# Performance work log

Hardware: AMD Instinct MI355X
Metric: run time of the kernel (lower is better)

## Reference

```python
import jax, jax.numpy as jnp
import numpy as np

START_IDX = 1


def lstm_cell(x, h, c, Wih, Whh, b):
    # x:[B,Din] h,c:[B,Hc]  Wih:[4Hc,Din] Whh:[4Hc,Hc] b:[4Hc] (b_ih+b_hh combined)
    gates = x @ Wih.T + h @ Whh.T + b
    i, f, g, o = jnp.split(gates, 4, axis=-1)
    c = jax.nn.sigmoid(f) * c + jax.nn.sigmoid(i) * jnp.tanh(g)
    h = jax.nn.sigmoid(o) * jnp.tanh(c)
    return h, c


def run_lstm_dir(xs, Wih, Whh, b, h0, c0, reverse):
    # xs:[T,B,Din] -> ys:[T,B,Hc] aligned with input positions (PyTorch semantics)
    def step(carry, x):
        h, c = carry
        h, c = lstm_cell(x, h, c, Wih, Whh, b)
        return (h, c), h
    (h, c), ys = jax.lax.scan(step, (h0, c0), xs, reverse=reverse)
    return ys, h, c


def encoder_forward(x, enc_emb, enc_Wih, enc_Whh, enc_b):
    B, T = x.shape
    L = enc_Wih.shape[0]
    H2 = enc_Whh.shape[-1]
    xs = enc_emb[x].transpose(1, 0, 2)  # [T,B,H]
    h_l, c_l = [], []
    for l in range(L):
        h0 = jnp.zeros((B, H2), xs.dtype)
        yf, hf, cf = run_lstm_dir(xs, enc_Wih[l, 0], enc_Whh[l, 0], enc_b[l, 0], h0, h0, False)
        yb, hb, cb = run_lstm_dir(xs, enc_Wih[l, 1], enc_Whh[l, 1], enc_b[l, 1], h0, h0, True)
        xs = jnp.concatenate([yf, yb], axis=-1)  # [T,B,H]
        h_l += [hf, hb]
        c_l += [cf, cb]
    # torch permute/reshape: per-layer hidden = concat(fwd, bwd) -> [L,B,H]
    hh = jnp.stack([jnp.concatenate([h_l[2 * l], h_l[2 * l + 1]], -1) for l in range(L)])
    cc = jnp.stack([jnp.concatenate([c_l[2 * l], c_l[2 * l + 1]], -1) for l in range(L)])
    return hh, cc


def decoder_forward(T, hh, cc, dec_emb, dec_Wih, dec_Whh, dec_b, clf_W, clf_b):
    L = dec_Wih.shape[0]

    def step(carry, _):
        hh, cc, tok = carry
        xt = dec_emb[tok][None, :]  # [1,H]
        nh, nc = [], []
        for l in range(L):
            h, c = lstm_cell(xt, hh[l], cc[l], dec_Wih[l], dec_Whh[l], dec_b[l])
            nh.append(h)
            nc.append(c)
            xt = h
        logits = xt[0] @ clf_W.T + clf_b  # [V]
        y = jax.nn.softmax(logits)
        tok = jnp.argmax(y).astype(jnp.int32)
        return (jnp.stack(nh), jnp.stack(nc), tok), y

    init = (hh, cc, jnp.asarray(START_IDX, jnp.int32))
    _, ys = jax.lax.scan(step, init, None, length=T)
    return ys  # [T,V]


def setup_inputs() -> dict:
    key = jax.random.key(0)
    ks = jax.random.split(key, 12)
    Vin, Vout, H, L, T, B = 32000, 32000, 1024, 2, 512, 1
    H2 = H // 2
    u = lambda k, shp, s: jax.random.uniform(k, shp, jnp.float32, -s, s)
    lstm_s = 1.0 / np.sqrt(H2)
    dec_s = 1.0 / np.sqrt(H)
    return {
        "x": jax.random.randint(ks[0], (B, T), 0, Vin),
        "enc_emb": 0.2 * jax.random.normal(ks[1], (Vin, H), jnp.float32),
        "enc_Wih": u(ks[2], (L, 2, 4 * H2, H), lstm_s),
        "enc_Whh": u(ks[3], (L, 2, 4 * H2, H2), lstm_s),
        "enc_b": u(ks[4], (L, 2, 4 * H2), lstm_s),
        "dec_emb": 0.2 * jax.random.normal(ks[5], (Vout, H), jnp.float32),
        "dec_Wih": u(ks[6], (L, 4 * H, H), dec_s),
        "dec_Whh": u(ks[7], (L, 4 * H, H), dec_s),
        "dec_b": u(ks[8], (L, 4 * H), dec_s),
        "clf_W": 0.2 * jax.random.normal(ks[9], (Vout, H), jnp.float32),
        "clf_b": u(ks[10], (Vout,), dec_s),
    }


def reference(x, enc_emb, enc_Wih, enc_Whh, enc_b, dec_emb, dec_Wih, dec_Whh, dec_b, clf_W, clf_b):
    T = x.shape[1]
    hh, cc = encoder_forward(x, enc_emb, enc_Wih, enc_Whh, enc_b)
    ys = decoder_forward(T, hh, cc, dec_emb, dec_Wih, dec_Whh, dec_b, clf_W, clf_b)  # [T,V]
    return ys.T[None]  # torch: stack(result).t().unsqueeze(0) -> [1,V,T]
```

## Files before the change

kernel.cpp:

```cpp
#include <hip/hip_runtime.h>
#include <stdint.h>
#include <math.h>

#define TT   512
#define HH_  1024
#define H2_  512
#define VV   32000
#define NB   256
#define BT   512

#define OF_XS0 16
#define OF_XS1 (OF_XS0 + TT*HH_)
#define OF_EH  (OF_XS1 + TT*HH_)
#define OF_EC  (OF_EH + 2048)
#define OF_HHF (OF_EC + 1024)
#define OF_CCF (OF_HHF + 2048)
#define OF_DH  (OF_CCF + 2048)
#define OF_DC  (OF_DH + 4096)
#define OF_LOG (OF_DC + 2048)

struct Ctl { int cnt; int gen; int pad[2]; unsigned long long slot[2]; };

__device__ __forceinline__ float wredsum(float v){
#pragma unroll
  for (int s = 32; s > 0; s >>= 1) v += __shfl_xor(v, s, 64);
  return v;
}
__device__ __forceinline__ float sigm(float x){ return 1.f/(1.f + __expf(-x)); }
__device__ __forceinline__ float tanh_(float x){
  float e = __expf(-2.f*fabsf(x));
  float t = (1.f - e)/(1.f + e);
  return copysignf(t, x);
}
__device__ __forceinline__ unsigned long long packmax(float v, int idx){
  unsigned u = __float_as_uint(v);
  u = (u & 0x80000000u) ? ~u : (u | 0x80000000u);
  return ((unsigned long long)u << 32) | (unsigned)(~idx);
}

__device__ __forceinline__ void gridbar(Ctl* c){
  __syncthreads();
  if (threadIdx.x == 0) {
    __builtin_amdgcn_fence(__ATOMIC_RELEASE, "agent");
    int g = __hip_atomic_load(&c->gen, __ATOMIC_RELAXED, __HIP_MEMORY_SCOPE_AGENT);
    int v = __hip_atomic_fetch_add(&c->cnt, 1, __ATOMIC_RELAXED, __HIP_MEMORY_SCOPE_AGENT);
    if (v == NB-1) {
      __hip_atomic_store(&c->cnt, 0, __ATOMIC_RELAXED, __HIP_MEMORY_SCOPE_AGENT);
      __hip_atomic_store(&c->gen, g+1, __ATOMIC_RELEASE, __HIP_MEMORY_SCOPE_AGENT);
    } else {
      while (__hip_atomic_load(&c->gen, __ATOMIC_RELAXED, __HIP_MEMORY_SCOPE_AGENT) == g)
        __builtin_amdgcn_s_sleep(1);
    }
    __builtin_amdgcn_fence(__ATOMIC_ACQUIRE, "agent");
  }
  __syncthreads();
}

__global__ __launch_bounds__(BT, 1) void seq2seq_k(
    const int*   __restrict__ x,
    const float* __restrict__ enc_emb,
    const float* __restrict__ enc_Wih,
    const float* __restrict__ enc_Whh,
    const float* __restrict__ enc_b,
    const float* __restrict__ dec_emb,
    const float* __restrict__ dec_Wih,
    const float* __restrict__ dec_Whh,
    const float* __restrict__ dec_b,
    const float* __restrict__ clf_W,
    const float* __restrict__ clf_b,
    float* __restrict__ ws)
{
  Ctl* ctl = (Ctl*)ws;
  const int blk = blockIdx.x, tid = threadIdx.x;
  const int wave = tid >> 6, lane = tid & 63;
  float* xs0 = ws + OF_XS0;
  float* xs1 = ws + OF_XS1;
  float* EH  = ws + OF_EH;
  float* EC  = ws + OF_EC;
  float* HHf = ws + OF_HHF;
  float* CCf = ws + OF_CCF;
  float* DH  = ws + OF_DH;
  float* DC  = ws + OF_DC;
  float* LG  = ws + OF_LOG;

  __shared__ float sg[4][2][4];
  __shared__ float cbv[8];
  __shared__ int   cbi[8];

  for (int i = blk*BT + tid; i < TT*HH_; i += NB*BT) {
    int t = i >> 10, d = i & 1023;
    xs0[i] = enc_emb[(size_t)x[t]*HH_ + d];
  }
  for (int i = blk*BT + tid; i < 3072; i += NB*BT) EH[i] = 0.f;
  gridbar(ctl);

  const float* xsrc = xs0;
#pragma unroll 1
  for (int l = 0; l < 2; ++l) {
    const float* Wih = enc_Wih + (size_t)l*2*2048*1024;
    const float* Whh = enc_Whh + (size_t)l*2*2048*512;
    const float* Bb  = enc_b  + l*2*2048;
#pragma unroll 1
    for (int s = 0; s < TT; ++s) {
      const int par = s & 1;
      {
        const int pl = wave >> 1, half = wave & 1;
        const int p = blk*4 + pl;
        const int dir = p >> 9, j = p & 511;
        const int t = dir ? (TT-1-s) : s;
        const float* xr = xsrc + (size_t)t*HH_;
        const float* hS = EH + par*1024 + dir*512;
        const float* wb = Wih + (size_t)dir*2048*1024;
        const float* hb = Whh + (size_t)dir*2048*512;
        float a0=0,a1=0,a2=0,a3=0;
#pragma unroll
        for (int it = 0; it < 8; ++it) {
          int k = it*128 + half*64 + lane;
          float xv = xr[k];
          a0 += wb[(size_t)(0*512+j)*1024 + k]*xv;
          a1 += wb[(size_t)(1*512+j)*1024 + k]*xv;
          a2 += wb[(size_t)(2*512+j)*1024 + k]*xv;
          a3 += wb[(size_t)(3*512+j)*1024 + k]*xv;
        }
#pragma unroll
        for (int it = 0; it < 4; ++it) {
          int k = it*128 + half*64 + lane;
          float hv = hS[k];
          a0 += hb[(size_t)(0*512+j)*512 + k]*hv;
          a1 += hb[(size_t)(1*512+j)*512 + k]*hv;
          a2 += hb[(size_t)(2*512+j)*512 + k]*hv;
          a3 += hb[(size_t)(3*512+j)*512 + k]*hv;
        }
        a0 = wredsum(a0); a1 = wredsum(a1); a2 = wredsum(a2); a3 = wredsum(a3);
        if (lane == 0) { sg[pl][half][0]=a0; sg[pl][half][1]=a1; sg[pl][half][2]=a2; sg[pl][half][3]=a3; }
      }
      __syncthreads();
      if (tid < 4) {
        const int p = blk*4 + tid;
        const int dir = p >> 9, j = p & 511;
        const int t = dir ? (TT-1-s) : s;
        float gi = sg[tid][0][0]+sg[tid][1][0] + Bb[dir*2048 + 0*512 + j];
        float gf = sg[tid][0][1]+sg[tid][1][1] + Bb[dir*2048 + 1*512 + j];
        float gg = sg[tid][0][2]+sg[tid][1][2] + Bb[dir*2048 + 2*512 + j];
        float go = sg[tid][0][3]+sg[tid][1][3] + Bb[dir*2048 + 3*512 + j];
        float c  = EC[dir*512 + j];
        float cn = sigm(gf)*c + sigm(gi)*tanh_(gg);
        float hn = sigm(go)*tanh_(cn);
        EC[dir*512 + j] = cn;
        EH[(par^1)*1024 + dir*512 + j] = hn;
        if (l == 0) xs1[(size_t)t*HH_ + dir*512 + j] = hn;
        if (s == TT-1) { HHf[l*1024 + dir*512 + j] = hn; CCf[l*1024 + dir*512 + j] = cn; }
      }
      gridbar(ctl);
    }
    if (l == 0) {
      for (int i = blk*BT + tid; i < 3072; i += NB*BT) EH[i] = 0.f;
      xsrc = xs1;
      gridbar(ctl);
    }
  }

  for (int i = blk*BT + tid; i < 2048; i += NB*BT) {
    int l = i >> 10, d = i & 1023;
    DH[(l*2 + 0)*1024 + d] = HHf[i];
    DH[(l*2 + 1)*1024 + d] = 0.f;
    DC[i] = CCf[i];
  }
  if (blk == 0 && tid == 0) { ctl->slot[0] = 0ull; ctl->slot[1] = 0ull; }
  gridbar(ctl);

#pragma unroll 1
  for (int t = 0; t < TT; ++t) {
    const int par = t & 1;
    int tok;
    if (t == 0) tok = 1;
    else {
      unsigned long long pk = __hip_atomic_load(&ctl->slot[(t-1)&1], __ATOMIC_RELAXED, __HIP_MEMORY_SCOPE_AGENT);
      tok = (int)(~(unsigned)(pk & 0xFFFFFFFFull));
    }
    const float* xt = dec_emb + (size_t)tok*HH_;

    {
      const float* Wih = dec_Wih;
      const float* Whh = dec_Whh;
      const float* hS  = DH + (0*2 + par)*1024;
      const int pl = wave >> 1, half = wave & 1;
      const int j = blk*4 + pl;
      float a0=0,a1=0,a2=0,a3=0;
#pragma unroll
      for (int it = 0; it < 8; ++it) {
        int k = it*128 + half*64 + lane;
        float xv = xt[k];
        a0 += Wih[(size_t)(0*1024+j)*1024 + k]*xv;
        a1 += Wih[(size_t)(1*1024+j)*1024 + k]*xv;
        a2 += Wih[(size_t)(2*1024+j)*1024 + k]*xv;
        a3 += Wih[(size_t)(3*1024+j)*1024 + k]*xv;
      }
#pragma unroll
      for (int it = 0; it < 8; ++it) {
        int k = it*128 + half*64 + lane;
        float hv = hS[k];
        a0 += Whh[(size_t)(0*1024+j)*1024 + k]*hv;
        a1 += Whh[(size_t)(1*1024+j)*1024 + k]*hv;
        a2 += Whh[(size_t)(2*1024+j)*1024 + k]*hv;
        a3 += Whh[(size_t)(3*1024+j)*1024 + k]*hv;
      }
      a0 = wredsum(a0); a1 = wredsum(a1); a2 = wredsum(a2); a3 = wredsum(a3);
      if (lane == 0) { sg[pl][half][0]=a0; sg[pl][half][1]=a1; sg[pl][half][2]=a2; sg[pl][half][3]=a3; }
      __syncthreads();
      if (tid < 4) {
        const int j2 = blk*4 + tid;
        float gi = sg[tid][0][0]+sg[tid][1][0] + dec_b[0*1024 + j2];
        float gf = sg[tid][0][1]+sg[tid][1][1] + dec_b[1*1024 + j2];
        float gg = sg[tid][0][2]+sg[tid][1][2] + dec_b[2*1024 + j2];
        float go = sg[tid][0][3]+sg[tid][1][3] + dec_b[3*1024 + j2];
        float c  = DC[j2];
        float cn = sigm(gf)*c + sigm(gi)*tanh_(gg);
        float hn = sigm(go)*tanh_(cn);
        DC[j2] = cn;
        DH[(0*2 + (par^1))*1024 + j2] = hn;
      }
    }
    gridbar(ctl);

    {
      const float* Wih = dec_Wih + (size_t)4096*1024;
      const float* Whh = dec_Whh + (size_t)4096*1024;
      const float* x2  = DH + (0*2 + (par^1))*1024;
      const float* hS  = DH + (1*2 + par)*1024;
      const int pl = wave >> 1, half = wave & 1;
      const int j = blk*4 + pl;
      float a0=0,a1=0,a2=0,a3=0;
#pragma unroll
      for (int it = 0; it < 8; ++it) {
        int k = it*128 + half*64 + lane;
        float xv = x2[k];
        a0 += Wih[(size_t)(0*1024+j)*1024 + k]*xv;
        a1 += Wih[(size_t)(1*1024+j)*1024 + k]*xv;
        a2 += Wih[(size_t)(2*1024+j)*1024 + k]*xv;
        a3 += Wih[(size_t)(3*1024+j)*1024 + k]*xv;
      }
#pragma unroll
      for (int it = 0; it < 8; ++it) {
        int k = it*128 + half*64 + lane;
        float hv = hS[k];
        a0 += Whh[(size_t)(0*1024+j)*1024 + k]*hv;
        a1 += Whh[(size_t)(1*1024+j)*1024 + k]*hv;
        a2 += Whh[(size_t)(2*1024+j)*1024 + k]*hv;
        a3 += Whh[(size_t)(3*1024+j)*1024 + k]*hv;
      }
      a0 = wredsum(a0); a1 = wredsum(a1); a2 = wredsum(a2); a3 = wredsum(a3);
      if (lane == 0) { sg[pl][half][0]=a0; sg[pl][half][1]=a1; sg[pl][half][2]=a2; sg[pl][half][3]=a3; }
      __syncthreads();
      if (tid < 4) {
        const int j2 = blk*4 + tid;
        float gi = sg[tid][0][0]+sg[tid][1][0] + dec_b[4096 + 0*1024 + j2];
        float gf = sg[tid][0][1]+sg[tid][1][1] + dec_b[4096 + 1*1024 + j2];
        float gg = sg[tid][0][2]+sg[tid][1][2] + dec_b[4096 + 2*1024 + j2];
        float go = sg[tid][0][3]+sg[tid][1][3] + dec_b[4096 + 3*1024 + j2];
        float c  = DC[1024 + j2];
        float cn = sigm(gf)*c + sigm(gi)*tanh_(gg);
        float hn = sigm(go)*tanh_(cn);
        DC[1024 + j2] = cn;
        DH[(1*2 + (par^1))*1024 + j2] = hn;
      }
      if (blk == 0 && tid == 0)
        __hip_atomic_store(&ctl->slot[(t+1)&1], 0ull, __ATOMIC_RELAXED, __HIP_MEMORY_SCOPE_AGENT);
    }
    gridbar(ctl);

    {
      const float* h2 = DH + (1*2 + (par^1))*1024;
      const int gw = blk*8 + wave;
      float bv = -INFINITY; int bi = 0;
#pragma unroll 1
      for (int i = 0; i < 16; ++i) {
        int row = gw + i*2048;
        if (row < VV) {
          const float* wr = clf_W + (size_t)row*1024;
          float a = 0.f;
#pragma unroll
          for (int it = 0; it < 16; ++it) { int k = it*64 + lane; a += wr[k]*h2[k]; }
          a = wredsum(a) + clf_b[row];
          if (lane == 0) LG[(size_t)t*VV + row] = a;
          if (a > bv) { bv = a; bi = row; }
        }
      }
      if (lane == 0) { cbv[wave] = bv; cbi[wave] = bi; }
      __syncthreads();
      if (tid == 0) {
        float v = cbv[0]; int ix = cbi[0];
#pragma unroll
        for (int w2 = 1; w2 < 8; ++w2) {
          float v2 = cbv[w2]; int i2 = cbi[w2];
          if (v2 > v || (v2 == v && i2 < ix)) { v = v2; ix = i2; }
        }
        atomicMax(&ctl->slot[t&1], packmax(v, ix));
      }
    }
    gridbar(ctl);
  }
}

__global__ __launch_bounds__(256, 1) void softmax_k(const float* __restrict__ LG, float* __restrict__ out){
  const int t = blockIdx.x, tid = threadIdx.x;
  __shared__ float red[256];
  const float* row = LG + (size_t)t*VV;
  float mx = -INFINITY;
  for (int v = tid; v < VV; v += 256) mx = fmaxf(mx, row[v]);
  red[tid] = mx; __syncthreads();
  for (int s = 128; s > 0; s >>= 1) { if (tid < s) red[tid] = fmaxf(red[tid], red[tid+s]); __syncthreads(); }
  mx = red[0]; __syncthreads();
  float sum = 0.f;
  for (int v = tid; v < VV; v += 256) sum += __expf(row[v]-mx);
  red[tid] = sum; __syncthreads();
  for (int s = 128; s > 0; s >>= 1) { if (tid < s) red[tid] += red[tid+s]; __syncthreads(); }
  float inv = 1.f/red[0];
  for (int v = tid; v < VV; v += 256) out[(size_t)v*TT + t] = __expf(row[v]-mx)*inv;
}

extern "C" void kernel_launch(void* const* d_in, const int* in_sizes, int n_in,
                              void* d_out, int out_size, void* d_ws, size_t ws_size,
                              hipStream_t stream) {
  const int*   x       = (const int*)d_in[0];
  const float* enc_emb = (const float*)d_in[1];
  const float* enc_Wih = (const float*)d_in[2];
  const float* enc_Whh = (const float*)d_in[3];
  const float* enc_b   = (const float*)d_in[4];
  const float* dec_emb = (const float*)d_in[5];
  const float* dec_Wih = (const float*)d_in[6];
  const float* dec_Whh = (const float*)d_in[7];
  const float* dec_b   = (const float*)d_in[8];
  const float* clf_W   = (const float*)d_in[9];
  const float* clf_b   = (const float*)d_in[10];
  float* ws = (float*)d_ws;

  hipMemsetAsync(d_ws, 0, 256, stream);
  hipLaunchKernelGGL(seq2seq_k, dim3(NB), dim3(BT), 0, stream,
                     x, enc_emb, enc_Wih, enc_Whh, enc_b,
                     dec_emb, dec_Wih, dec_Whh, dec_b, clf_W, clf_b, ws);
  hipLaunchKernelGGL(softmax_k, dim3(TT), dim3(256), 0, stream,
                     ws + OF_LOG, (float*)d_out);
}
```

Before: 47.43 ms.

## Cache LSTM weights in LDS, use flag-based grid barrier, keep cell state in registers

Each block now loads its slice of the encoder weights, and later the decoder layer-0 weights, into 128KB of shared memory once. Every timestep then reads them from LDS with float4 loads instead of streaming them from global memory. The single-counter atomic grid barrier becomes a flag/generation barrier in which block 0 polls a per-block flag and then releases everyone. Cell states and biases stay in registers, and the classifier dot products use float4 loads with four rows in flight. The cost is a large LDS allocation, a larger control region that must be zeroed, and a barrier serialised through block 0.

```diff
diff --git a/kernel.cpp b/kernel.cpp
--- a/kernel.cpp
+++ b/kernel.cpp
@@ -4,22 +4,18 @@
 
 #define TT   512
 #define HH_  1024
-#define H2_  512
 #define VV   32000
 #define NB   256
 #define BT   512
 
-#define OF_XS0 16
+#define CTRL_BYTES 17408
+#define OF_XS0 4352
 #define OF_XS1 (OF_XS0 + TT*HH_)
 #define OF_EH  (OF_XS1 + TT*HH_)
-#define OF_EC  (OF_EH + 2048)
-#define OF_HHF (OF_EC + 1024)
+#define OF_HHF (OF_EH + 2048)
 #define OF_CCF (OF_HHF + 2048)
 #define OF_DH  (OF_CCF + 2048)
-#define OF_DC  (OF_DH + 4096)
-#define OF_LOG (OF_DC + 2048)
-
-struct Ctl { int cnt; int gen; int pad[2]; unsigned long long slot[2]; };
+#define OF_LOG (OF_DH + 4096)
 
 __device__ __forceinline__ float wredsum(float v){
 #pragma unroll
@@ -38,22 +34,25 @@
   return ((unsigned long long)u << 32) | (unsigned)(~idx);
 }
 
-__device__ __forceinline__ void gridbar(Ctl* c){
+__device__ __forceinline__ void gridbar(int* gen, int* flags, int g){
   __syncthreads();
-  if (threadIdx.x == 0) {
-    __builtin_amdgcn_fence(__ATOMIC_RELEASE, "agent");
-    int g = __hip_atomic_load(&c->gen, __ATOMIC_RELAXED, __HIP_MEMORY_SCOPE_AGENT);
-    int v = __hip_atomic_fetch_add(&c->cnt, 1, __ATOMIC_RELAXED, __HIP_MEMORY_SCOPE_AGENT);
-    if (v == NB-1) {
-      __hip_atomic_store(&c->cnt, 0, __ATOMIC_RELAXED, __HIP_MEMORY_SCOPE_AGENT);
-      __hip_atomic_store(&c->gen, g+1, __ATOMIC_RELEASE, __HIP_MEMORY_SCOPE_AGENT);
-    } else {
-      while (__hip_atomic_load(&c->gen, __ATOMIC_RELAXED, __HIP_MEMORY_SCOPE_AGENT) == g)
+  if (blockIdx.x == 0) {
+    const int t = threadIdx.x;
+    if (t >= 1 && t < NB) {
+      while (__hip_atomic_load(&flags[t*16], __ATOMIC_ACQUIRE, __HIP_MEMORY_SCOPE_AGENT) < g)
         __builtin_amdgcn_s_sleep(1);
     }
-    __builtin_amdgcn_fence(__ATOMIC_ACQUIRE, "agent");
-  }
-  __syncthreads();
+    __syncthreads();
+    if (t == 0)
+      __hip_atomic_store(gen, g, __ATOMIC_RELEASE, __HIP_MEMORY_SCOPE_AGENT);
+  } else {
+    if (threadIdx.x == 0) {
+      __hip_atomic_store(&flags[blockIdx.x*16], g, __ATOMIC_RELEASE, __HIP_MEMORY_SCOPE_AGENT);
+      while (__hip_atomic_load(gen, __ATOMIC_ACQUIRE, __HIP_MEMORY_SCOPE_AGENT) < g)
+        __builtin_amdgcn_s_sleep(4);
+    }
+    __syncthreads();
+  }
 }
 
 __global__ __launch_bounds__(BT, 1) void seq2seq_k(
@@ -70,223 +69,262 @@
     const float* __restrict__ clf_b,
     float* __restrict__ ws)
 {
-  Ctl* ctl = (Ctl*)ws;
   const int blk = blockIdx.x, tid = threadIdx.x;
   const int wave = tid >> 6, lane = tid & 63;
+  int* genp = (int*)ws;
+  unsigned long long* slots = (unsigned long long*)((char*)ws + 8);
+  int* flags = (int*)((char*)ws + 1024);
   float* xs0 = ws + OF_XS0;
   float* xs1 = ws + OF_XS1;
   float* EH  = ws + OF_EH;
-  float* EC  = ws + OF_EC;
   float* HHf = ws + OF_HHF;
   float* CCf = ws + OF_CCF;
   float* DH  = ws + OF_DH;
-  float* DC  = ws + OF_DC;
   float* LG  = ws + OF_LOG;
 
+  __shared__ float lds[32768];
   __shared__ float sg[4][2][4];
   __shared__ float cbv[8];
   __shared__ int   cbi[8];
-
-  for (int i = blk*BT + tid; i < TT*HH_; i += NB*BT) {
-    int t = i >> 10, d = i & 1023;
-    xs0[i] = enc_emb[(size_t)x[t]*HH_ + d];
-  }
-  for (int i = blk*BT + tid; i < 3072; i += NB*BT) EH[i] = 0.f;
-  gridbar(ctl);
+  __shared__ int   stok;
+
+  int bgen = 0;
+#define GB() do { ++bgen; gridbar(genp, flags, bgen); } while(0)
+
+  {
+    const float4* emb4 = (const float4*)enc_emb;
+    float4* xs04 = (float4*)xs0;
+    for (int i4 = blk*BT + tid; i4 < TT*256; i4 += NB*BT) {
+      int t = i4 >> 8, d4 = i4 & 255;
+      xs04[i4] = emb4[(size_t)x[t]*256 + d4];
+    }
+    for (int i = blk*BT + tid; i < 2048; i += NB*BT) EH[i] = 0.f;
+  }
+  GB();
 
   const float* xsrc = xs0;
 #pragma unroll 1
   for (int l = 0; l < 2; ++l) {
     const float* Wih = enc_Wih + (size_t)l*2*2048*1024;
     const float* Whh = enc_Whh + (size_t)l*2*2048*512;
-    const float* Bb  = enc_b  + l*2*2048;
+    __syncthreads();
+#pragma unroll 1
+    for (int pl = 0; pl < 4; ++pl) {
+      const int p = blk*4 + pl, dir = p >> 9, j = p & 511;
+      const float* wbase = Wih + (size_t)dir*2048*1024;
+      const float* hbase = Whh + (size_t)dir*2048*512;
+#pragma unroll 1
+      for (int g = 0; g < 4; ++g) {
+        float* dst = lds + pl*6144 + g*1536;
+        const float* s1 = wbase + (size_t)(g*512 + j)*1024;
+        for (int k = tid; k < 1024; k += BT) dst[k] = s1[k];
+        const float* s2 = hbase + (size_t)(g*512 + j)*512;
+        for (int k = tid; k < 512; k += BT) dst[1024 + k] = s2[k];
+      }
+    }
+    const int pe = blk*4 + (tid & 3), dire = pe >> 9, je = pe & 511;
+    const float* Bb = enc_b + l*2*2048 + dire*2048;
+    float bi_ = Bb[je], bf_ = Bb[512 + je], bg_ = Bb[1024 + je], bo_ = Bb[1536 + je];
+    float creg = 0.f;
+    __syncthreads();
+
 #pragma unroll 1
     for (int s = 0; s < TT; ++s) {
       const int par = s & 1;
       {
         const int pl = wave >> 1, half = wave & 1;
-        const int p = blk*4 + pl;
-        const int dir = p >> 9, j = p & 511;
+        const int p = blk*4 + pl, dir = p >> 9;
         const int t = dir ? (TT-1-s) : s;
-        const float* xr = xsrc + (size_t)t*HH_;
-        const float* hS = EH + par*1024 + dir*512;
-        const float* wb = Wih + (size_t)dir*2048*1024;
-        const float* hb = Whh + (size_t)dir*2048*512;
-        float a0=0,a1=0,a2=0,a3=0;
-#pragma unroll
-        for (int it = 0; it < 8; ++it) {
-          int k = it*128 + half*64 + lane;
-          float xv = xr[k];
-          a0 += wb[(size_t)(0*512+j)*1024 + k]*xv;
-          a1 += wb[(size_t)(1*512+j)*1024 + k]*xv;
-          a2 += wb[(size_t)(2*512+j)*1024 + k]*xv;
-          a3 += wb[(size_t)(3*512+j)*1024 + k]*xv;
+        const float4* xr4 = (const float4*)(xsrc + (size_t)t*HH_);
+        const float4* h4  = (const float4*)(EH + par*1024 + dir*512);
+        float4 xv0 = xr4[half*128 + lane];
+        float4 xv1 = xr4[half*128 + 64 + lane];
+        float4 hv  = h4[half*64 + lane];
+        const float* wl = lds + pl*6144;
+        float acc[4];
+#pragma unroll
+        for (int g = 0; g < 4; ++g) {
+          const float4* wv = (const float4*)(wl + g*1536);
+          const float4* wh = (const float4*)(wl + g*1536 + 1024);
+          float4 wa = wv[half*128 + lane];
+          float4 wb = wv[half*128 + 64 + lane];
+          float4 wc = wh[half*64 + lane];
+          acc[g] = wa.x*xv0.x + wa.y*xv0.y + wa.z*xv0.z + wa.w*xv0.w
+                 + wb.x*xv1.x + wb.y*xv1.y + wb.z*xv1.z + wb.w*xv1.w
+                 + wc.x*hv.x  + wc.y*hv.y  + wc.z*hv.z  + wc.w*hv.w;
         }
 #pragma unroll
-        for (int it = 0; it < 4; ++it) {
-          int k = it*128 + half*64 + lane;
-          float hv = hS[k];
-          a0 += hb[(size_t)(0*512+j)*512 + k]*hv;
-          a1 += hb[(size_t)(1*512+j)*512 + k]*hv;
-          a2 += hb[(size_t)(2*512+j)*512 + k]*hv;
-          a3 += hb[(size_t)(3*512+j)*512 + k]*hv;
-        }
-        a0 = wredsum(a0); a1 = wredsum(a1); a2 = wredsum(a2); a3 = wredsum(a3);
-        if (lane == 0) { sg[pl][half][0]=a0; sg[pl][half][1]=a1; sg[pl][half][2]=a2; sg[pl][half][3]=a3; }
+        for (int g = 0; g < 4; ++g) acc[g] = wredsum(acc[g]);
+        if (lane == 0) { sg[pl][half][0]=acc[0]; sg[pl][half][1]=acc[1]; sg[pl][half][2]=acc[2]; sg[pl][half][3]=acc[3]; }
       }
       __syncthreads();
       if (tid < 4) {
-        const int p = blk*4 + tid;
-        const int dir = p >> 9, j = p & 511;
-        const int t = dir ? (TT-1-s) : s;
-        float gi = sg[tid][0][0]+sg[tid][1][0] + Bb[dir*2048 + 0*512 + j];
-        float gf = sg[tid][0][1]+sg[tid][1][1] + Bb[dir*2048 + 1*512 + j];
-        float gg = sg[tid][0][2]+sg[tid][1][2] + Bb[dir*2048 + 2*512 + j];
-        float go = sg[tid][0][3]+sg[tid][1][3] + Bb[dir*2048 + 3*512 + j];
-        float c  = EC[dir*512 + j];
-        float cn = sigm(gf)*c + sigm(gi)*tanh_(gg);
+        float gi = sg[tid][0][0]+sg[tid][1][0] + bi_;
+        float gf = sg[tid][0][1]+sg[tid][1][1] + bf_;
+        float gg = sg[tid][0][2]+sg[tid][1][2] + bg_;
+        float go = sg[tid][0][3]+sg[tid][1][3] + bo_;
+        float cn = sigm(gf)*creg + sigm(gi)*tanh_(gg);
         float hn = sigm(go)*tanh_(cn);
-        EC[dir*512 + j] = cn;
-        EH[(par^1)*1024 + dir*512 + j] = hn;
-        if (l == 0) xs1[(size_t)t*HH_ + dir*512 + j] = hn;
-        if (s == TT-1) { HHf[l*1024 + dir*512 + j] = hn; CCf[l*1024 + dir*512 + j] = cn; }
-      }
-      gridbar(ctl);
+        creg = cn;
+        const int te = dire ? (TT-1-s) : s;
+        EH[(par^1)*1024 + dire*512 + je] = hn;
+        if (l == 0) xs1[(size_t)te*HH_ + dire*512 + je] = hn;
+        if (s == TT-1) { HHf[l*1024 + dire*512 + je] = hn; CCf[l*1024 + dire*512 + je] = cn; }
+      }
+      GB();
     }
     if (l == 0) {
-      for (int i = blk*BT + tid; i < 3072; i += NB*BT) EH[i] = 0.f;
+      for (int i = blk*BT + tid; i < 2048; i += NB*BT) EH[i] = 0.f;
       xsrc = xs1;
-      gridbar(ctl);
+      GB();
     }
   }
 
   for (int i = blk*BT + tid; i < 2048; i += NB*BT) {
-    int l = i >> 10, d = i & 1023;
-    DH[(l*2 + 0)*1024 + d] = HHf[i];
-    DH[(l*2 + 1)*1024 + d] = 0.f;
-    DC[i] = CCf[i];
-  }
-  if (blk == 0 && tid == 0) { ctl->slot[0] = 0ull; ctl->slot[1] = 0ull; }
-  gridbar(ctl);
+    int l2 = i >> 10, d = i & 1023;
+    DH[(l2*2 + 0)*1024 + d] = HHf[i];
+    DH[(l2*2 + 1)*1024 + d] = 0.f;
+  }
+  if (blk == 0 && tid == 0) {
+    __hip_atomic_store(&slots[0], 0ull, __ATOMIC_RELAXED, __HIP_MEMORY_SCOPE_AGENT);
+    __hip_atomic_store(&slots[1], 0ull, __ATOMIC_RELAXED, __HIP_MEMORY_SCOPE_AGENT);
+  }
+  __syncthreads();
+#pragma unroll 1
+  for (int pl = 0; pl < 4; ++pl) {
+    const int j = blk*4 + pl;
+#pragma unroll 1
+    for (int g = 0; g < 4; ++g) {
+      float* dst = lds + pl*8192 + g*2048;
+      const float* s1 = dec_Wih + (size_t)(g*1024 + j)*1024;
+      for (int k = tid; k < 1024; k += BT) dst[k] = s1[k];
+      const float* s2 = dec_Whh + (size_t)(g*1024 + j)*1024;
+      for (int k = tid; k < 1024; k += BT) dst[1024 + k] = s2[k];
+    }
+  }
+  const int j2 = blk*4 + (tid & 3);
+  const float b0i = dec_b[j2],        b0f = dec_b[1024 + j2],        b0g = dec_b[2048 + j2],        b0o = dec_b[3072 + j2];
+  const float b1i = dec_b[4096 + j2], b1f = dec_b[4096 + 1024 + j2], b1g = dec_b[4096 + 2048 + j2], b1o = dec_b[4096 + 3072 + j2];
+  float c0reg = CCf[j2], c1reg = CCf[1024 + j2];
+  GB();
 
 #pragma unroll 1
   for (int t = 0; t < TT; ++t) {
     const int par = t & 1;
-    int tok;
-    if (t == 0) tok = 1;
-    else {
-      unsigned long long pk = __hip_atomic_load(&ctl->slot[(t-1)&1], __ATOMIC_RELAXED, __HIP_MEMORY_SCOPE_AGENT);
-      tok = (int)(~(unsigned)(pk & 0xFFFFFFFFull));
-    }
-    const float* xt = dec_emb + (size_t)tok*HH_;
+    if (tid == 0) {
+      int tk = 1;
+      if (t > 0) {
+        unsigned long long pk = __hip_atomic_load(&slots[(t-1)&1], __ATOMIC_RELAXED, __HIP_MEMORY_SCOPE_AGENT);
+        tk = (int)(~(unsigned)(pk & 0xFFFFFFFFull));
+      }
+      stok = tk;
+    }
+    __syncthreads();
+    const int tok = stok;
+    const int pl = wave >> 1, half = wave & 1;
 
     {
-      const float* Wih = dec_Wih;
-      const float* Whh = dec_Whh;
-      const float* hS  = DH + (0*2 + par)*1024;
-      const int pl = wave >> 1, half = wave & 1;
-      const int j = blk*4 + pl;
-      float a0=0,a1=0,a2=0,a3=0;
-#pragma unroll
-      for (int it = 0; it < 8; ++it) {
-        int k = it*128 + half*64 + lane;
-        float xv = xt[k];
-        a0 += Wih[(size_t)(0*1024+j)*1024 + k]*xv;
-        a1 += Wih[(size_t)(1*1024+j)*1024 + k]*xv;
-        a2 += Wih[(size_t)(2*1024+j)*1024 + k]*xv;
-        a3 += Wih[(size_t)(3*1024+j)*1024 + k]*xv;
-      }
-#pragma unroll
-      for (int it = 0; it < 8; ++it) {
-        int k = it*128 + half*64 + lane;
-        float hv = hS[k];
-        a0 += Whh[(size_t)(0*1024+j)*1024 + k]*hv;
-        a1 += Whh[(size_t)(1*1024+j)*1024 + k]*hv;
-        a2 += Whh[(size_t)(2*1024+j)*1024 + k]*hv;
-        a3 += Whh[(size_t)(3*1024+j)*1024 + k]*hv;
-      }
-      a0 = wredsum(a0); a1 = wredsum(a1); a2 = wredsum(a2); a3 = wredsum(a3);
-      if (lane == 0) { sg[pl][half][0]=a0; sg[pl][half][1]=a1; sg[pl][half][2]=a2; sg[pl][half][3]=a3; }
+      const float* vsrc = half ? (DH + (0*2 + par)*1024) : (dec_emb + (size_t)tok*1024);
+      const float4* z4 = (const float4*)vsrc;
+      float4 zv0 = z4[lane], zv1 = z4[64+lane], zv2 = z4[128+lane], zv3 = z4[192+lane];
+      const float* wl = lds + pl*8192 + half*1024;
+      float acc[4];
+#pragma unroll
+      for (int g = 0; g < 4; ++g) {
+        const float4* w4 = (const float4*)(wl + g*2048);
+        float4 w0 = w4[lane], w1 = w4[64+lane], w2 = w4[128+lane], w3 = w4[192+lane];
+        acc[g] = w0.x*zv0.x+w0.y*zv0.y+w0.z*zv0.z+w0.w*zv0.w
+               + w1.x*zv1.x+w1.y*zv1.y+w1.z*zv1.z+w1.w*zv1.w
+               + w2.x*zv2.x+w2.y*zv2.y+w2.z*zv2.z+w2.w*zv2.w
+               + w3.x*zv3.x+w3.y*zv3.y+w3.z*zv3.z+w3.w*zv3.w;
+      }
+#pragma unroll
+      for (int g = 0; g < 4; ++g) acc[g] = wredsum(acc[g]);
+      if (lane == 0) { sg[pl][half][0]=acc[0]; sg[pl][half][1]=acc[1]; sg[pl][half][2]=acc[2]; sg[pl][half][3]=acc[3]; }
       __syncthreads();
       if (tid < 4) {
-        const int j2 = blk*4 + tid;
-        float gi = sg[tid][0][0]+sg[tid][1][0] + dec_b[0*1024 + j2];
-        float gf = sg[tid][0][1]+sg[tid][1][1] + dec_b[1*1024 + j2];
-        float gg = sg[tid][0][2]+sg[tid][1][2] + dec_b[2*1024 + j2];
-        float go = sg[tid][0][3]+sg[tid][1][3] + dec_b[3*1024 + j2];
-        float c  = DC[j2];
-        float cn = sigm(gf)*c + sigm(gi)*tanh_(gg);
+        float gi = sg[tid][0][0]+sg[tid][1][0] + b0i;
+        float gf = sg[tid][0][1]+sg[tid][1][1] + b0f;
+        float gg = sg[tid][0][2]+sg[tid][1][2] + b0g;
+        float go = sg[tid][0][3]+sg[tid][1][3] + b0o;
+        float cn = sigm(gf)*c0reg + sigm(gi)*tanh_(gg);
         float hn = sigm(go)*tanh_(cn);
-        DC[j2] = cn;
+        c0reg = cn;
         DH[(0*2 + (par^1))*1024 + j2] = hn;
       }
     }
-    gridbar(ctl);
+    GB();
 
     {
-      const float* Wih = dec_Wih + (size_t)4096*1024;
-      const float* Whh = dec_Whh + (size_t)4096*1024;
-      const float* x2  = DH + (0*2 + (par^1))*1024;
-      const float* hS  = DH + (1*2 + par)*1024;
-      const int pl = wave >> 1, half = wave & 1;
+      const float* Wih1 = dec_Wih + (size_t)4096*1024;
+      const float* Whh1 = dec_Whh + (size_t)4096*1024;
+      const float* vsrc = half ? (DH + (1*2 + par)*1024) : (DH + (0*2 + (par^1))*1024);
+      const float* wsrc = half ? Whh1 : Wih1;
       const int j = blk*4 + pl;
-      float a0=0,a1=0,a2=0,a3=0;
-#pragma unroll
-      for (int it = 0; it < 8; ++it) {
-        int k = it*128 + half*64 + lane;
-        float xv = x2[k];
-        a0 += Wih[(size_t)(0*1024+j)*1024 + k]*xv;
-        a1 += Wih[(size_t)(1*1024+j)*1024 + k]*xv;
-        a2 += Wih[(size_t)(2*1024+j)*1024 + k]*xv;
-        a3 += Wih[(size_t)(3*1024+j)*1024 + k]*xv;
-      }
-#pragma unroll
-      for (int it = 0; it < 8; ++it) {
-        int k = it*128 + half*64 + lane;
-        float hv = hS[k];
-        a0 += Whh[(size_t)(0*1024+j)*1024 + k]*hv;
-        a1 += Whh[(size_t)(1*1024+j)*1024 + k]*hv;
-        a2 += Whh[(size_t)(2*1024+j)*1024 + k]*hv;
-        a3 += Whh[(size_t)(3*1024+j)*1024 + k]*hv;
-      }
-      a0 = wredsum(a0); a1 = wredsum(a1); a2 = wredsum(a2); a3 = wredsum(a3);
-      if (lane == 0) { sg[pl][half][0]=a0; sg[pl][half][1]=a1; sg[pl][half][2]=a2; sg[pl][half][3]=a3; }
+      const float4* z4 = (const float4*)vsrc;
+      float4 zv0 = z4[lane], zv1 = z4[64+lane], zv2 = z4[128+lane], zv3 = z4[192+lane];
+      float acc[4];
+#pragma unroll
+      for (int g = 0; g < 4; ++g) {
+        const float4* w4 = (const float4*)(wsrc + (size_t)(g*1024 + j)*1024);
+        float4 w0 = w4[lane], w1 = w4[64+lane], w2 = w4[128+lane], w3 = w4[192+lane];
+        acc[g] = w0.x*zv0.x+w0.y*zv0.y+w0.z*zv0.z+w0.w*zv0.w
+               + w1.x*zv1.x+w1.y*zv1.y+w1.z*zv1.z+w1.w*zv1.w
+               + w2.x*zv2.x+w2.y*zv2.y+w2.z*zv2.z+w2.w*zv2.w
+               + w3.x*zv3.x+w3.y*zv3.y+w3.z*zv3.z+w3.w*zv3.w;
+      }
+#pragma unroll
+      for (int g = 0; g < 4; ++g) acc[g] = wredsum(acc[g]);
+      if (lane == 0) { sg[pl][half][0]=acc[0]; sg[pl][half][1]=acc[1]; sg[pl][half][2]=acc[2]; sg[pl][half][3]=acc[3]; }
       __syncthreads();
       if (tid < 4) {
-        const int j2 = blk*4 + tid;
-        float gi = sg[tid][0][0]+sg[tid][1][0] + dec_b[4096 + 0*1024 + j2];
-        float gf = sg[tid][0][1]+sg[tid][1][1] + dec_b[4096 + 1*1024 + j2];
-        float gg = sg[tid][0][2]+sg[tid][1][2] + dec_b[4096 + 2*1024 + j2];
-        float go = sg[tid][0][3]+sg[tid][1][3] + dec_b[4096 + 3*1024 + j2];
-        float c  = DC[1024 + j2];
-        float cn = sigm(gf)*c + sigm(gi)*tanh_(gg);
+        float gi = sg[tid][0][0]+sg[tid][1][0] + b1i;
+        float gf = sg[tid][0][1]+sg[tid][1][1] + b1f;
+        float gg = sg[tid][0][2]+sg[tid][1][2] + b1g;
+        float go = sg[tid][0][3]+sg[tid][1][3] + b1o;
+        float cn = sigm(gf)*c1reg + sigm(gi)*tanh_(gg);
         float hn = sigm(go)*tanh_(cn);
-        DC[1024 + j2] = cn;
+        c1reg = cn;
         DH[(1*2 + (par^1))*1024 + j2] = hn;
       }
       if (blk == 0 && tid == 0)
-        __hip_atomic_store(&ctl->slot[(t+1)&1], 0ull, __ATOMIC_RELAXED, __HIP_MEMORY_SCOPE_AGENT);
-    }
-    gridbar(ctl);
+        __hip_atomic_store(&slots[(t+1)&1], 0ull, __ATOMIC_RELAXED, __HIP_MEMORY_SCOPE_AGENT);
+    }
+    GB();
 
     {
       const float* h2 = DH + (1*2 + (par^1))*1024;
+      const float4* h4 = (const float4*)h2;
+      float4 hv0 = h4[lane], hv1 = h4[64+lane], hv2 = h4[128+lane], hv3 = h4[192+lane];
       const int gw = blk*8 + wave;
-      float bv = -INFINITY; int bi = 0;
-#pragma unroll 1
-      for (int i = 0; i < 16; ++i) {
-        int row = gw + i*2048;
-        if (row < VV) {
-          const float* wr = clf_W + (size_t)row*1024;
-          float a = 0.f;
-#pragma unroll
-          for (int it = 0; it < 16; ++it) { int k = it*64 + lane; a += wr[k]*h2[k]; }
-          a = wredsum(a) + clf_b[row];
-          if (lane == 0) LG[(size_t)t*VV + row] = a;
-          if (a > bv) { bv = a; bi = row; }
+      float bv = -INFINITY; int bix = 0;
+#pragma unroll 1
+      for (int ii = 0; ii < 4; ++ii) {
+        float a4[4];
+#pragma unroll
+        for (int r = 0; r < 4; ++r) {
+          const int row = gw + (ii*4 + r)*2048;
+          a4[r] = 0.f;
+          if (row < VV) {
+            const float4* w4 = (const float4*)(clf_W + (size_t)row*1024);
+            float4 w0 = w4[lane], w1 = w4[64+lane], w2 = w4[128+lane], w3 = w4[192+lane];
+            a4[r] = w0.x*hv0.x+w0.y*hv0.y+w0.z*hv0.z+w0.w*hv0.w
+                  + w1.x*hv1.x+w1.y*hv1.y+w1.z*hv1.z+w1.w*hv1.w
+                  + w2.x*hv2.x+w2.y*hv2.y+w2.z*hv2.z+w2.w*hv2.w
+                  + w3.x*hv3.x+w3.y*hv3.y+w3.z*hv3.z+w3.w*hv3.w;
+          }
         }
-      }
-      if (lane == 0) { cbv[wave] = bv; cbi[wave] = bi; }
+#pragma unroll
+        for (int r = 0; r < 4; ++r) {
+          const int row = gw + (ii*4 + r)*2048;
+          if (row < VV) {
+            float a = wredsum(a4[r]) + clf_b[row];
+            if (lane == 0) LG[(size_t)t*VV + row] = a;
+            if (a > bv) { bv = a; bix = row; }
+          }
+        }
+      }
+      if (lane == 0) { cbv[wave] = bv; cbi[wave] = bix; }
       __syncthreads();
       if (tid == 0) {
         float v = cbv[0]; int ix = cbi[0];
@@ -295,11 +333,12 @@
           float v2 = cbv[w2]; int i2 = cbi[w2];
           if (v2 > v || (v2 == v && i2 < ix)) { v = v2; ix = i2; }
         }
-        atomicMax(&ctl->slot[t&1], packmax(v, ix));
-      }
-    }
-    gridbar(ctl);
-  }
+        atomicMax(&slots[t&1], packmax(v, ix));
+      }
+    }
+    GB();
+  }
+#undef GB
 }
 
 __global__ __launch_bounds__(256, 1) void softmax_k(const float* __restrict__ LG, float* __restrict__ out){
@@ -335,7 +374,7 @@
   const float* clf_b   = (const float*)d_in[10];
   float* ws = (float*)d_ws;
 
-  hipMemsetAsync(d_ws, 0, 256, stream);
+  hipMemsetAsync(d_ws, 0, CTRL_BYTES, stream);
   hipLaunchKernelGGL(seq2seq_k, dim3(NB), dim3(BT), 0, stream,
                      x, enc_emb, enc_Wih, enc_Whh, enc_b,
                      dec_emb, dec_Wih, dec_Whh, dec_b, clf_W, clf_b, ws);
```

Result: slower. 75.05 ms (+58.2%).
